# Kernel optimization log

Measured on AMD Instinct MI355X. Metric: run time of the kernel, lower is better.

## Reference

```python
import jax, jax.numpy as jnp
import numpy as np

N = 50000
E = 800000
D = 128

def setup_inputs() -> dict:
    key = jax.random.key(0)
    ks = jax.random.split(key, 10)
    s = 1.0 / np.sqrt(D)
    return {
        "hidden": jax.random.normal(ks[0], (N, D), dtype=jnp.float32),
        "edge_index": jax.random.randint(ks[1], (2, E), 0, N, dtype=jnp.int64),
        "edge_attr": jax.random.uniform(ks[2], (E, 1), dtype=jnp.float32),
        # edge_encoder: Linear(1, D)
        "We": jax.random.uniform(ks[3], (1, D), minval=-1.0, maxval=1.0, dtype=jnp.float32),
        "be": jax.random.uniform(ks[4], (D,), minval=-1.0, maxval=1.0, dtype=jnp.float32),
        # mlp: Linear(D,D) -> ReLU -> Linear(D,D); weights stored [in,out]
        "W1": jax.random.uniform(ks[5], (D, D), minval=-s, maxval=s, dtype=jnp.float32),
        "b1": jax.random.uniform(ks[6], (D,), minval=-s, maxval=s, dtype=jnp.float32),
        "W2": jax.random.uniform(ks[7], (D, D), minval=-s, maxval=s, dtype=jnp.float32),
        "b2": jax.random.uniform(ks[8], (D,), minval=-s, maxval=s, dtype=jnp.float32),
        "eps": jnp.zeros((1,), dtype=jnp.float32),
    }

def reference(hidden, edge_index, edge_attr, We, be, W1, b1, W2, b2, eps):
    # NOTE: original forward computes relu(hidden) but discards it, passing
    # raw `hidden` into the conv; replicated faithfully.
    src, dst = edge_index[0], edge_index[1]
    edge_emb = edge_attr @ We + be                      # [E, D]
    msg = jax.nn.relu(hidden[src] + edge_emb)           # gather + message
    summed = jax.ops.segment_sum(msg, dst, num_segments=N)           # [N, D]
    cnt = jax.ops.segment_sum(jnp.ones((E,), hidden.dtype), dst, num_segments=N)
    aggr = summed / jnp.maximum(cnt, 1.0)[:, None]      # scatter-mean
    h = (1.0 + eps[0]) * hidden + aggr
    h = jax.nn.relu(h @ W1 + b1)
    out = h @ W2 + b2
    return out
```

## Files before the change

kernel.cpp:

```cpp
#include <hip/hip_runtime.h>

static constexpr int N_NODES = 50000;
static constexpr int D = 128;
static constexpr int E_EDGES = 800000;
static constexpr int SLOTS = 48;
static constexpr int TILES = N_NODES / 16;

static constexpr int BKW  = 192;
static constexpr int NB   = (N_NODES + BKW - 1) / BKW;
static constexpr int CAP  = 4096;
static constexpr int EPB  = 4096;
static constexpr int ABIN = (E_EDGES + EPB - 1) / EPB;
static constexpr int ACVT = (E_EDGES + 511) / 512;
static constexpr int AWPR = 8;

using half8   = __attribute__((ext_vector_type(8))) _Float16;
using half2v  = __attribute__((ext_vector_type(2))) _Float16;
using floatx4 = __attribute__((ext_vector_type(4))) float;

__global__ __launch_bounds__(512) void bin_coarse(
    const float* __restrict__ hidden,
    const int* __restrict__ edge_index,
    const float* __restrict__ edge_attr,
    const float* __restrict__ W1, const float* __restrict__ W2,
    _Float16* __restrict__ hidden16,
    _Float16* __restrict__ W1f, _Float16* __restrict__ W2f,
    int* __restrict__ bucketFill, int2* __restrict__ coarse)
{
    const int t = threadIdx.x;
    const int b = blockIdx.x;

    if (b >= ABIN + ACVT) {
        int p = (b - ABIN - ACVT) * 512 + t;
        int lane  = p & 63;
        int ntile = (p >> 6) & 7;
        int kstep = (p >> 9) & 3;
        int mat   = p >> 11;
        const float* W = mat ? W2 : W1;
        _Float16*   Wf = mat ? W2f : W1f;
        int n     = ntile * 16 + (lane & 15);
        int kbase = kstep * 32 + (lane >> 4) * 8;
        _Float16* dst = Wf + ((size_t)((kstep * 8 + ntile) * 64 + lane)) * 8;
        #pragma unroll
        for (int j = 0; j < 8; ++j)
            dst[j] = (_Float16)W[(size_t)(kbase + j) * D + n];
        return;
    }
    if (b >= ABIN) {
        int e = (b - ABIN) * 512 + t;
        if (e < N_NODES * D / 8) {
            float4 v0 = *((const float4*)hidden + 2 * (size_t)e);
            float4 v1 = *((const float4*)hidden + 2 * (size_t)e + 1);
            half8 o;
            o[0] = (_Float16)v0.x; o[1] = (_Float16)v0.y;
            o[2] = (_Float16)v0.z; o[3] = (_Float16)v0.w;
            o[4] = (_Float16)v1.x; o[5] = (_Float16)v1.y;
            o[6] = (_Float16)v1.z; o[7] = (_Float16)v1.w;
            ((half8*)hidden16)[e] = o;
        }
        return;
    }

    __shared__ int lcnt[NB];
    __shared__ int lbase[NB];
    if (t < NB) lcnt[t] = 0;
    __syncthreads();

    const int ebase = b * EPB;
    int src[8], bk[8], dl[8], rank[8];
    float at[8];
    #pragma unroll
    for (int k = 0; k < 8; ++k) {
        int e = ebase + k * 512 + t;
        bool v = e < E_EDGES;
        int d  = v ? edge_index[E_EDGES + e] : 0;
        src[k] = v ? edge_index[e] : 0;
        at[k]  = v ? edge_attr[e] : 0.f;
        bk[k]  = (int)((unsigned)d / (unsigned)BKW);
        dl[k]  = d - bk[k] * BKW;
        rank[k] = v ? 0 : -1;
    }
    #pragma unroll
    for (int k = 0; k < 8; ++k)
        if (rank[k] >= 0)
            rank[k] = atomicAdd(&lcnt[bk[k]], 1);
    __syncthreads();

    if (t < NB) {
        int c = lcnt[t];
        lbase[t] = (c > 0) ? atomicAdd(&bucketFill[t], c) : 0;
    }
    __syncthreads();

    #pragma unroll
    for (int k = 0; k < 8; ++k) {
        if (rank[k] >= 0) {
            int idx = lbase[bk[k]] + rank[k];
            if (idx < CAP)
                coarse[(size_t)bk[k] * CAP + idx] =
                    make_int2(src[k] | (dl[k] << 16), __float_as_int(at[k]));
        }
    }
}

__global__ __launch_bounds__(512) void bin_fine(
    const int2* __restrict__ coarse,
    const int* __restrict__ bucketFill,
    int* __restrict__ counts, int2* __restrict__ csr)
{
    __shared__ int2 tile[BKW * SLOTS];
    __shared__ int  lcnt[BKW];
    const int t  = threadIdx.x;
    const int b  = blockIdx.x;
    const int n0 = b * BKW;
    const int nn = min(N_NODES - n0, BKW);

    int4* tz = (int4*)tile;
    for (int i = t; i < BKW * SLOTS / 2; i += 512)
        tz[i] = make_int4(0, 0, 0, 0);
    if (t < BKW) lcnt[t] = 0;
    __syncthreads();

    const int cnt = min(__builtin_amdgcn_readfirstlane(bucketFill[b]), CAP);
    const int2* seg = coarse + (size_t)b * CAP;
    for (int r = t; r < cnt; r += 512) {
        int2 rec = seg[r];
        int d   = (rec.x >> 16) & 0xff;
        int pos = atomicAdd(&lcnt[d], 1);
        if (pos < SLOTS)
            tile[d * SLOTS + pos] = make_int2(rec.x & 0xffff, rec.y);
    }
    __syncthreads();

    int4* gout = (int4*)(csr + (size_t)n0 * SLOTS);
    const int4* tin = (const int4*)tile;
    const int nq = nn * SLOTS / 2;
    for (int i = t; i < nq; i += 512)
        gout[i] = tin[i];
    if (t < nn) counts[n0 + t] = lcnt[t];
}

__global__ __launch_bounds__(512) void fused_gather_mlp(
    const _Float16* __restrict__ hidden16,
    const int2* __restrict__ csr,
    const int* __restrict__ counts,
    const float* __restrict__ We, const float* __restrict__ be,
    const float* __restrict__ eps,
    const _Float16* __restrict__ W1f, const float* __restrict__ b1,
    const _Float16* __restrict__ W2f, const float* __restrict__ b2,
    float* __restrict__ out)
{
    __shared__ _Float16 hA[16 * 136];
    __shared__ _Float16 tB[16 * 136];
    const int tid  = threadIdx.x;
    const int wave = tid >> 6;
    const int lane = tid & 63;
    const int node0 = blockIdx.x * 16;
    const int d0 = lane << 1;

    const float2 wv = *(const float2*)(We + d0);
    const float2 bv = *(const float2*)(be + d0);
    const float onePlusEps = 1.0f + eps[0];

    const int nbase = node0 + __builtin_amdgcn_readfirstlane(wave << 1);
    const int2 c2 = *(const int2*)(counts + nbase);
    int dg[2];
    dg[0] = c2.x; dg[1] = c2.y;

    int m_[2];
    const int2* ep[2];
    #pragma unroll
    for (int i = 0; i < 2; ++i) {
        m_[i] = min(dg[i], SLOTS);
        ep[i] = csr + (size_t)(nbase + i) * SLOTS;
    }
    float a0[2] = {0.f, 0.f};
    float a1[2] = {0.f, 0.f};
    const int mmax = max(m_[0], m_[1]);

    for (int j = 0; j < mmax; j += 4) {
        #pragma unroll
        for (int u = 0; u < 4; ++u) {
            #pragma unroll
            for (int i = 0; i < 2; ++i) {
                int2 rec = ep[i][j + u];
                int   src = rec.x;
                float at  = __int_as_float(rec.y);
                const float g = ((j + u) < m_[i]) ? 1.0f : 0.0f;
                half2v hp = *(const half2v*)(hidden16 + ((size_t)src << 7) + d0);
                float t0 = fmaxf((float)hp.x + __builtin_fmaf(at, wv.x, bv.x), 0.f);
                float t1 = fmaxf((float)hp.y + __builtin_fmaf(at, wv.y, bv.y), 0.f);
                a0[i] = __builtin_fmaf(g, t0, a0[i]);
                a1[i] = __builtin_fmaf(g, t1, a1[i]);
            }
        }
    }

    #pragma unroll
    for (int i = 0; i < 2; ++i) {
        const int row = (nbase - node0) + i;
        const float rin = 1.0f / fmaxf((float)dg[i], 1.0f);
        half2v hidp = *(const half2v*)(hidden16 + (size_t)(nbase + i) * D + d0);
        half2v o;
        o.x = (_Float16)(onePlusEps * (float)hidp.x + a0[i] * rin);
        o.y = (_Float16)(onePlusEps * (float)hidp.y + a1[i] * rin);
        *(half2v*)&hA[row * 136 + d0] = o;
    }
    __syncthreads();

    const int ln16 = lane & 15;
    const int quad = lane >> 4;
    const int nt   = wave;

    half8 a[4];
    #pragma unroll
    for (int ks = 0; ks < 4; ++ks)
        a[ks] = *(const half8*)&hA[ln16 * 136 + ks * 32 + quad * 8];

    floatx4 acc;
    {
        float bb = b1[nt * 16 + ln16];
        acc = (floatx4){bb, bb, bb, bb};
        #pragma unroll
        for (int ks = 0; ks < 4; ++ks) {
            half8 b = *(const half8*)(W1f + ((size_t)((ks * 8 + nt) * 64 + lane)) * 8);
            acc = __builtin_amdgcn_mfma_f32_16x16x32_f16(a[ks], b, acc, 0, 0, 0);
        }
    }
    #pragma unroll
    for (int r = 0; r < 4; ++r)
        tB[(quad * 4 + r) * 136 + nt * 16 + ln16] = (_Float16)fmaxf(acc[r], 0.f);
    __syncthreads();

    #pragma unroll
    for (int ks = 0; ks < 4; ++ks)
        a[ks] = *(const half8*)&tB[ln16 * 136 + ks * 32 + quad * 8];

    {
        float bb = b2[nt * 16 + ln16];
        acc = (floatx4){bb, bb, bb, bb};
        #pragma unroll
        for (int ks = 0; ks < 4; ++ks) {
            half8 b = *(const half8*)(W2f + ((size_t)((ks * 8 + nt) * 64 + lane)) * 8);
            acc = __builtin_amdgcn_mfma_f32_16x16x32_f16(a[ks], b, acc, 0, 0, 0);
        }
    }
    #pragma unroll
    for (int r = 0; r < 4; ++r)
        __builtin_nontemporal_store(
            acc[r], &out[(size_t)(node0 + quad * 4 + r) * D + nt * 16 + ln16]);
}

extern "C" void kernel_launch(void* const* d_in, const int* in_sizes, int n_in,
                              void* d_out, int out_size, void* d_ws, size_t ws_size,
                              hipStream_t stream) {
    const float* hidden     = (const float*)d_in[0];
    const int*   edge_index = (const int*)d_in[1];
    const float* edge_attr  = (const float*)d_in[2];
    const float* We         = (const float*)d_in[3];
    const float* be         = (const float*)d_in[4];
    const float* W1         = (const float*)d_in[5];
    const float* b1         = (const float*)d_in[6];
    const float* W2         = (const float*)d_in[7];
    const float* b2         = (const float*)d_in[8];
    const float* eps        = (const float*)d_in[9];
    float* out = (float*)d_out;

    _Float16* hidden16   = (_Float16*)d_ws;
    _Float16* W1f        = hidden16 + (size_t)N_NODES * D;
    _Float16* W2f        = W1f + (size_t)D * D;
    int*      counts     = (int*)(W2f + (size_t)D * D);
    int2*     csr        = (int2*)(counts + N_NODES);
    int*      bucketFill = (int*)(csr + (size_t)N_NODES * SLOTS);
    int2*     coarse     = (int2*)(bucketFill + 272);

    hipMemsetAsync(bucketFill, 0, NB * sizeof(int), stream);

    bin_coarse<<<ABIN + ACVT + AWPR, 512, 0, stream>>>(
        hidden, edge_index, edge_attr, W1, W2, hidden16, W1f, W2f,
        bucketFill, coarse);

    bin_fine<<<NB, 512, 0, stream>>>(coarse, bucketFill, counts, csr);

    fused_gather_mlp<<<TILES, 512, 0, stream>>>(
        hidden16, csr, counts, We, be, eps, W1f, b1, W2f, b2, out);
}
```

Measured before the change: 150.5 us.

## Fuse fine binning into gather-MLP kernel, dropping the CSR intermediate

Removes the bin_fine kernel and its global CSR/counts buffers. Each 16-node tile block now scans its whole coarse bucket, keeps records whose destination falls in its tile, and builds a small per-tile edge list in shared memory. The gather then reads edges from LDS with scalar broadcasts. This removes one launch and a large CSR write/read, but each bucket's coarse data is rescanned by 12 blocks.

```diff
diff --git a/kernel.cpp b/kernel.cpp
--- a/kernel.cpp
+++ b/kernel.cpp
@@ -103,89 +103,71 @@
     }
 }
 
-__global__ __launch_bounds__(512) void bin_fine(
+__global__ __launch_bounds__(512) void fused_gather_mlp(
+    const _Float16* __restrict__ hidden16,
     const int2* __restrict__ coarse,
     const int* __restrict__ bucketFill,
-    int* __restrict__ counts, int2* __restrict__ csr)
-{
-    __shared__ int2 tile[BKW * SLOTS];
-    __shared__ int  lcnt[BKW];
-    const int t  = threadIdx.x;
-    const int b  = blockIdx.x;
-    const int n0 = b * BKW;
-    const int nn = min(N_NODES - n0, BKW);
-
-    int4* tz = (int4*)tile;
-    for (int i = t; i < BKW * SLOTS / 2; i += 512)
-        tz[i] = make_int4(0, 0, 0, 0);
-    if (t < BKW) lcnt[t] = 0;
-    __syncthreads();
-
-    const int cnt = min(__builtin_amdgcn_readfirstlane(bucketFill[b]), CAP);
-    const int2* seg = coarse + (size_t)b * CAP;
-    for (int r = t; r < cnt; r += 512) {
-        int2 rec = seg[r];
-        int d   = (rec.x >> 16) & 0xff;
-        int pos = atomicAdd(&lcnt[d], 1);
-        if (pos < SLOTS)
-            tile[d * SLOTS + pos] = make_int2(rec.x & 0xffff, rec.y);
-    }
-    __syncthreads();
-
-    int4* gout = (int4*)(csr + (size_t)n0 * SLOTS);
-    const int4* tin = (const int4*)tile;
-    const int nq = nn * SLOTS / 2;
-    for (int i = t; i < nq; i += 512)
-        gout[i] = tin[i];
-    if (t < nn) counts[n0 + t] = lcnt[t];
-}
-
-__global__ __launch_bounds__(512) void fused_gather_mlp(
-    const _Float16* __restrict__ hidden16,
-    const int2* __restrict__ csr,
-    const int* __restrict__ counts,
     const float* __restrict__ We, const float* __restrict__ be,
     const float* __restrict__ eps,
     const _Float16* __restrict__ W1f, const float* __restrict__ b1,
     const _Float16* __restrict__ W2f, const float* __restrict__ b2,
     float* __restrict__ out)
 {
+    __shared__ int2 tile[16 * SLOTS];
+    __shared__ int  hcnt[16];
     __shared__ _Float16 hA[16 * 136];
     __shared__ _Float16 tB[16 * 136];
     const int tid  = threadIdx.x;
     const int wave = tid >> 6;
     const int lane = tid & 63;
     const int node0 = blockIdx.x * 16;
+    const int bkt  = node0 / BKW;
+    const int loc0 = node0 - bkt * BKW;
     const int d0 = lane << 1;
 
     const float2 wv = *(const float2*)(We + d0);
     const float2 bv = *(const float2*)(be + d0);
     const float onePlusEps = 1.0f + eps[0];
 
-    const int nbase = node0 + __builtin_amdgcn_readfirstlane(wave << 1);
-    const int2 c2 = *(const int2*)(counts + nbase);
-    int dg[2];
-    dg[0] = c2.x; dg[1] = c2.y;
-
-    int m_[2];
-    const int2* ep[2];
-    #pragma unroll
-    for (int i = 0; i < 2; ++i) {
-        m_[i] = min(dg[i], SLOTS);
-        ep[i] = csr + (size_t)(nbase + i) * SLOTS;
-    }
+    {
+        int4* tz = (int4*)tile;
+        if (tid < 384) tz[tid] = make_int4(0, 0, 0, 0);
+        if (tid < 16) hcnt[tid] = 0;
+    }
+    __syncthreads();
+
+    const int cnt = min(__builtin_amdgcn_readfirstlane(bucketFill[bkt]), CAP);
+    const int2* seg = coarse + (size_t)bkt * CAP;
+    for (int r = tid; r < cnt; r += 512) {
+        int2 rec = seg[r];
+        int row = ((rec.x >> 16) & 0xff) - loc0;
+        if ((unsigned)row < 16u) {
+            int pos = atomicAdd(&hcnt[row], 1);
+            if (pos < SLOTS)
+                tile[row * SLOTS + pos] = make_int2(rec.x & 0xffff, rec.y);
+        }
+    }
+    __syncthreads();
+
+    const int r0w = __builtin_amdgcn_readfirstlane(wave << 1);
+    int dg[2], m_[2];
+    dg[0] = __builtin_amdgcn_readfirstlane(hcnt[r0w]);
+    dg[1] = __builtin_amdgcn_readfirstlane(hcnt[r0w + 1]);
+    m_[0] = min(dg[0], SLOTS);
+    m_[1] = min(dg[1], SLOTS);
+    const int mmax = max(m_[0], m_[1]);
+
     float a0[2] = {0.f, 0.f};
     float a1[2] = {0.f, 0.f};
-    const int mmax = max(m_[0], m_[1]);
-
     for (int j = 0; j < mmax; j += 4) {
         #pragma unroll
         for (int u = 0; u < 4; ++u) {
             #pragma unroll
             for (int i = 0; i < 2; ++i) {
-                int2 rec = ep[i][j + u];
-                int   src = rec.x;
-                float at  = __int_as_float(rec.y);
+                int2 rec = tile[(r0w + i) * SLOTS + j + u];
+                int   src = __builtin_amdgcn_readfirstlane(rec.x);
+                float at  = __uint_as_float(
+                                (unsigned)__builtin_amdgcn_readfirstlane(rec.y));
                 const float g = ((j + u) < m_[i]) ? 1.0f : 0.0f;
                 half2v hp = *(const half2v*)(hidden16 + ((size_t)src << 7) + d0);
                 float t0 = fmaxf((float)hp.x + __builtin_fmaf(at, wv.x, bv.x), 0.f);
@@ -198,9 +180,9 @@
 
     #pragma unroll
     for (int i = 0; i < 2; ++i) {
-        const int row = (nbase - node0) + i;
+        const int row = r0w + i;
         const float rin = 1.0f / fmaxf((float)dg[i], 1.0f);
-        half2v hidp = *(const half2v*)(hidden16 + (size_t)(nbase + i) * D + d0);
+        half2v hidp = *(const half2v*)(hidden16 + (size_t)(node0 + row) * D + d0);
         half2v o;
         o.x = (_Float16)(onePlusEps * (float)hidp.x + a0[i] * rin);
         o.y = (_Float16)(onePlusEps * (float)hidp.y + a1[i] * rin);
@@ -269,9 +251,7 @@
     _Float16* hidden16   = (_Float16*)d_ws;
     _Float16* W1f        = hidden16 + (size_t)N_NODES * D;
     _Float16* W2f        = W1f + (size_t)D * D;
-    int*      counts     = (int*)(W2f + (size_t)D * D);
-    int2*     csr        = (int2*)(counts + N_NODES);
-    int*      bucketFill = (int*)(csr + (size_t)N_NODES * SLOTS);
+    int*      bucketFill = (int*)(W2f + (size_t)D * D);
     int2*     coarse     = (int2*)(bucketFill + 272);
 
     hipMemsetAsync(bucketFill, 0, NB * sizeof(int), stream);
@@ -280,8 +260,6 @@
         hidden, edge_index, edge_attr, W1, W2, hidden16, W1f, W2f,
         bucketFill, coarse);
 
-    bin_fine<<<NB, 512, 0, stream>>>(coarse, bucketFill, counts, csr);
-
     fused_gather_mlp<<<TILES, 512, 0, stream>>>(
-        hidden16, csr, counts, We, be, eps, W1f, b1, W2f, b2, out);
+        hidden16, coarse, bucketFill, We, be, eps, W1f, b1, W2f, b2, out);
 }
```

New measurement: 152.7 us. No clear change (+1.5%).
